# Optimization experiments

Measured on AMD Instinct MI355X. Metric: run time of the kernel, lower is better.

The kernel has to match this reference:

```python
import jax, jax.numpy as jnp
import numpy as np

WINDOW_SIZE = 16
DILATION = 2

B, L, H, E = 2, 4096, 8, 64


def setup_inputs() -> dict:
    key = jax.random.key(0)
    kq, kk, kv = jax.random.split(key, 3)
    queries = jax.random.normal(kq, (B, L, H, E), dtype=jnp.float32)
    keys = jax.random.normal(kk, (B, L, H, E), dtype=jnp.float32)
    values = jax.random.normal(kv, (B, L, H, E), dtype=jnp.float32)
    return {"queries": queries, "keys": keys, "values": values}


def _window_indices(Lk: int):
    # offsets: [-r, ..., r] * dilation ; idx[l, w] = clamp(l + off[w], 0, Lk-1)
    offsets = jnp.arange(-WINDOW_SIZE, WINDOW_SIZE + 1) * DILATION
    idx = jnp.arange(Lk)[:, None] + offsets[None, :]
    return jnp.clip(idx, 0, Lk - 1)


def reference(queries, keys, values):
    # queries/keys/values: [B, L, H, E]
    Bq, Lq, Hq, Eq = queries.shape
    scale = 1.0 / jnp.sqrt(jnp.asarray(Eq, queries.dtype))
    idx = _window_indices(keys.shape[1])
    K_win = keys[:, idx]
    V_win = values[:, idx]
    scores = jnp.einsum('blhe,blwhe->blhw', queries, K_win) * scale
    A = jax.nn.softmax(scores, axis=-1)
    V = jnp.einsum('blhw,blwhe->blhe', A, V_win)    # [B, L, H, E]
    return V
```

## Files before the change

### kernel.cpp

```cpp
#include <hip/hip_runtime.h>
#include <hip/hip_bf16.h>
#include <math.h>

#define B_    2
#define L_    4096
#define H_    8
#define E_    64
#define VTSTR 136
#define PSTR  72

using frag8 = __attribute__((ext_vector_type(8))) short;
using fl4   = __attribute__((ext_vector_type(4))) float;

__device__ __forceinline__ unsigned short f2bf(float f) {
    return __builtin_bit_cast(unsigned short, __float2bfloat16(f));
}
__device__ __forceinline__ frag8 pack8(float4 a, float4 b) {
    frag8 r;
    r[0] = (short)f2bf(a.x); r[1] = (short)f2bf(a.y);
    r[2] = (short)f2bf(a.z); r[3] = (short)f2bf(a.w);
    r[4] = (short)f2bf(b.x); r[5] = (short)f2bf(b.y);
    r[6] = (short)f2bf(b.z); r[7] = (short)f2bf(b.w);
    return r;
}

__global__ __launch_bounds__(256, 4)
void lda_kernel(const float* __restrict__ Q, const float* __restrict__ K,
                const float* __restrict__ V, float* __restrict__ O) {
    __shared__ unsigned short Vt[E_ * VTSTR];
    __shared__ unsigned short Pw[4 * 16 * PSTR];

    const int tid  = threadIdx.x;
    const int lane = tid & 63;
    const int wave = tid >> 6;
    const int col  = lane & 15;
    const int quad = lane >> 4;
    const int p    = wave & 1;
    const int t    = wave >> 1;

    const int g   = blockIdx.x;
    const int xcd = g & 7;
    const int s   = g >> 3;
    const int bh  = s & 15;
    const int xt  = (xcd << 3) | (s >> 4);
    const int l0  = xt * 64;
    const int b   = bh >> 3;
    const int h   = bh & 7;

    const size_t base = ((size_t)(b * L_) * H_ + h) * E_;
    const int    rs   = H_ * E_;

    const int lq = l0 + 2 * (16 * t + col) + p;
    frag8 aq[2];
    #pragma unroll
    for (int k = 0; k < 2; ++k) {
        const float* qp = Q + base + (size_t)lq * rs + k * 32 + quad * 8;
        aq[k] = pack8(*(const float4*)qp, *(const float4*)(qp + 4));
    }

    fl4 S[3];
    #pragma unroll
    for (int c = 0; c < 3; ++c) {
        int rhat = 16 * (t + c) + col;
        int rg = l0 - 32 + 2 * rhat + p;
        rg = rg < 0 ? 0 : (rg > L_ - 1 ? L_ - 1 : rg);
        const float* kp = K + base + (size_t)rg * rs;
        fl4 acc = {0.f, 0.f, 0.f, 0.f};
        #pragma unroll
        for (int k = 0; k < 2; ++k) {
            frag8 bk = pack8(*(const float4*)(kp + k * 32 + quad * 8),
                             *(const float4*)(kp + k * 32 + quad * 8 + 4));
            acc = __builtin_amdgcn_mfma_f32_16x16x32_bf16(aq[k], bk, acc, 0, 0, 0);
        }
        S[c] = acc;
    }

    float va[32];
    #pragma unroll
    for (int i = 0; i < 8; ++i) {
        int gi  = wave * 8 + i;
        int pg  = gi >> 4;
        int rh0 = (gi & 15) * 4;
        #pragma unroll
        for (int j = 0; j < 4; ++j) {
            int rg = l0 - 32 + 2 * (rh0 + j) + pg;
            rg = rg < 0 ? 0 : (rg > L_ - 1 ? L_ - 1 : rg);
            va[i * 4 + j] = V[base + (size_t)rg * rs + lane];
        }
    }

    float pw[3][4];
    #pragma unroll
    for (int c = 0; c < 3; ++c)
        #pragma unroll
        for (int reg = 0; reg < 4; ++reg)
            pw[c][reg] = exp2f(S[c][reg] * 0.18033688011112043f);

    const int pb = wave * 16 * PSTR;
    #pragma unroll
    for (int i = 0; i < 3; ++i) {
        int idx = lane + 64 * i;
        if (idx < 144) { uint4 z = {0u,0u,0u,0u}; *(uint4*)&Pw[pb + idx * 8] = z; }
    }
    #pragma unroll
    for (int reg = 0; reg < 4; ++reg) {
        int off = quad * 4 + reg;
        #pragma unroll
        for (int c = 0; c < 3; ++c) {
            int j = 16 * c + col - off;
            if (j >= 0 && j <= 32)
                Pw[pb + off * PSTR + 16 * (t + c) + col] = f2bf(pw[c][reg]);
        }
    }

    frag8 ap[2];
    #pragma unroll
    for (int k = 0; k < 2; ++k)
        ap[k] = *(const frag8*)&Pw[pb + col * PSTR + k * 32 + quad * 8];

    frag8 ones;
    #pragma unroll
    for (int i = 0; i < 8; ++i) ones[i] = (short)0x3F80;
    fl4 sums = {0.f, 0.f, 0.f, 0.f};
    sums = __builtin_amdgcn_mfma_f32_16x16x32_bf16(ap[0], ones, sums, 0, 0, 0);
    sums = __builtin_amdgcn_mfma_f32_16x16x32_bf16(ap[1], ones, sums, 0, 0, 0);
    float inv[4];
    #pragma unroll
    for (int reg = 0; reg < 4; ++reg) inv[reg] = __builtin_amdgcn_rcpf(sums[reg]);

    #pragma unroll
    for (int i = 0; i < 8; ++i) {
        int gi  = wave * 8 + i;
        int pg  = gi >> 4;
        int rh0 = (gi & 15) * 4;
        uint2 u;
        u.x = (unsigned)f2bf(va[i*4+0]) | ((unsigned)f2bf(va[i*4+1]) << 16);
        u.y = (unsigned)f2bf(va[i*4+2]) | ((unsigned)f2bf(va[i*4+3]) << 16);
        *(uint2*)&Vt[lane * VTSTR + pg * 64 + rh0] = u;
    }
    __syncthreads();

    #pragma unroll
    for (int nt = 0; nt < 4; ++nt) {
        fl4 c = {0.f, 0.f, 0.f, 0.f};
        #pragma unroll
        for (int k = 0; k < 2; ++k) {
            frag8 bv = *(const frag8*)&Vt[(nt * 16 + col) * VTSTR + p * 64 + k * 32 + quad * 8];
            c = __builtin_amdgcn_mfma_f32_16x16x32_bf16(ap[k], bv, c, 0, 0, 0);
        }
        #pragma unroll
        for (int reg = 0; reg < 4; ++reg) {
            int l = 2 * (16 * t + quad * 4 + reg) + p;
            __builtin_nontemporal_store(c[reg] * inv[reg],
                O + base + (size_t)(l0 + l) * rs + nt * 16 + col);
        }
    }
}

extern "C" void kernel_launch(void* const* d_in, const int* in_sizes, int n_in,
                              void* d_out, int out_size, void* d_ws, size_t ws_size,
                              hipStream_t stream) {
    const float* Q = (const float*)d_in[0];
    const float* K = (const float*)d_in[1];
    const float* V = (const float*)d_in[2];
    float* O = (float*)d_out;

    dim3 grid(L_ / 64 * B_ * H_);
    dim3 block(256);
    lda_kernel<<<grid, block, 0, stream>>>(Q, K, V, O);
}
```

Before: 91.80 us.

## Double block tile to 128 rows with 512 threads to cut V halo reloads

```diff
diff --git a/kernel.cpp b/kernel.cpp
--- a/kernel.cpp
+++ b/kernel.cpp
@@ -6,7 +6,7 @@
 #define L_    4096
 #define H_    8
 #define E_    64
-#define VTSTR 136
+#define VTSTR 200
 #define PSTR  72
 
 using frag8 = __attribute__((ext_vector_type(8))) short;
@@ -15,7 +15,7 @@
 __device__ __forceinline__ unsigned short f2bf(float f) {
     return __builtin_bit_cast(unsigned short, __float2bfloat16(f));
 }
-__device__ __forceinline__ frag8 pack8(float4 a, float4 b) {
+__device__ __forceinline__ frag8 pack8v(fl4 a, fl4 b) {
     frag8 r;
     r[0] = (short)f2bf(a.x); r[1] = (short)f2bf(a.y);
     r[2] = (short)f2bf(a.z); r[3] = (short)f2bf(a.w);
@@ -24,11 +24,11 @@
     return r;
 }
 
-__global__ __launch_bounds__(256, 4)
+__global__ __launch_bounds__(512, 2)
 void lda_kernel(const float* __restrict__ Q, const float* __restrict__ K,
                 const float* __restrict__ V, float* __restrict__ O) {
     __shared__ unsigned short Vt[E_ * VTSTR];
-    __shared__ unsigned short Pw[4 * 16 * PSTR];
+    __shared__ unsigned short Pw[8 * 16 * PSTR];
 
     const int tid  = threadIdx.x;
     const int lane = tid & 63;
@@ -42,8 +42,8 @@
     const int xcd = g & 7;
     const int s   = g >> 3;
     const int bh  = s & 15;
-    const int xt  = (xcd << 3) | (s >> 4);
-    const int l0  = xt * 64;
+    const int xt  = (xcd << 2) | (s >> 4);
+    const int l0  = xt * 128;
     const int b   = bh >> 3;
     const int h   = bh & 7;
 
@@ -55,7 +55,9 @@
     #pragma unroll
     for (int k = 0; k < 2; ++k) {
         const float* qp = Q + base + (size_t)lq * rs + k * 32 + quad * 8;
-        aq[k] = pack8(*(const float4*)qp, *(const float4*)(qp + 4));
+        fl4 qa = __builtin_nontemporal_load((const fl4*)qp);
+        fl4 qb = __builtin_nontemporal_load((const fl4*)qp + 1);
+        aq[k] = pack8v(qa, qb);
     }
 
     fl4 S[3];
@@ -68,19 +70,20 @@
         fl4 acc = {0.f, 0.f, 0.f, 0.f};
         #pragma unroll
         for (int k = 0; k < 2; ++k) {
-            frag8 bk = pack8(*(const float4*)(kp + k * 32 + quad * 8),
-                             *(const float4*)(kp + k * 32 + quad * 8 + 4));
+            frag8 bk = pack8v(*(const fl4*)(kp + k * 32 + quad * 8),
+                              *(const fl4*)(kp + k * 32 + quad * 8 + 4));
             acc = __builtin_amdgcn_mfma_f32_16x16x32_bf16(aq[k], bk, acc, 0, 0, 0);
         }
         S[c] = acc;
     }
 
-    float va[32];
+    float va[24];
     #pragma unroll
-    for (int i = 0; i < 8; ++i) {
-        int gi  = wave * 8 + i;
-        int pg  = gi >> 4;
-        int rh0 = (gi & 15) * 4;
+    for (int i = 0; i < 6; ++i) {
+        int gi  = wave * 6 + i;
+        int pg  = gi / 24;
+        int rm  = gi - pg * 24;
+        int rh0 = rm * 4;
         #pragma unroll
         for (int j = 0; j < 4; ++j) {
             int rg = l0 - 32 + 2 * (rh0 + j) + pg;
@@ -97,6 +100,7 @@
             pw[c][reg] = exp2f(S[c][reg] * 0.18033688011112043f);
 
     const int pb = wave * 16 * PSTR;
+    const int lb = 16 * (t & 1);
     #pragma unroll
     for (int i = 0; i < 3; ++i) {
         int idx = lane + 64 * i;
@@ -109,7 +113,7 @@
         for (int c = 0; c < 3; ++c) {
             int j = 16 * c + col - off;
             if (j >= 0 && j <= 32)
-                Pw[pb + off * PSTR + 16 * (t + c) + col] = f2bf(pw[c][reg]);
+                Pw[pb + off * PSTR + lb + 16 * c + col] = f2bf(pw[c][reg]);
         }
     }
 
@@ -129,30 +133,32 @@
     for (int reg = 0; reg < 4; ++reg) inv[reg] = __builtin_amdgcn_rcpf(sums[reg]);
 
     #pragma unroll
-    for (int i = 0; i < 8; ++i) {
-        int gi  = wave * 8 + i;
-        int pg  = gi >> 4;
-        int rh0 = (gi & 15) * 4;
+    for (int i = 0; i < 6; ++i) {
+        int gi  = wave * 6 + i;
+        int pg  = gi / 24;
+        int rm  = gi - pg * 24;
+        int rh0 = rm * 4;
         uint2 u;
         u.x = (unsigned)f2bf(va[i*4+0]) | ((unsigned)f2bf(va[i*4+1]) << 16);
         u.y = (unsigned)f2bf(va[i*4+2]) | ((unsigned)f2bf(va[i*4+3]) << 16);
-        *(uint2*)&Vt[lane * VTSTR + pg * 64 + rh0] = u;
+        *(uint2*)&Vt[lane * VTSTR + pg * 96 + rh0] = u;
     }
     __syncthreads();
 
+    const int rb = 32 * (t >> 1);
     #pragma unroll
     for (int nt = 0; nt < 4; ++nt) {
         fl4 c = {0.f, 0.f, 0.f, 0.f};
         #pragma unroll
         for (int k = 0; k < 2; ++k) {
-            frag8 bv = *(const frag8*)&Vt[(nt * 16 + col) * VTSTR + p * 64 + k * 32 + quad * 8];
+            frag8 bv = *(const frag8*)&Vt[(nt * 16 + col) * VTSTR + p * 96 + rb + k * 32 + quad * 8];
             c = __builtin_amdgcn_mfma_f32_16x16x32_bf16(ap[k], bv, c, 0, 0, 0);
         }
         #pragma unroll
         for (int reg = 0; reg < 4; ++reg) {
-            int l = 2 * (16 * t + quad * 4 + reg) + p;
+            int l = l0 + 2 * (16 * t + quad * 4 + reg) + p;
             __builtin_nontemporal_store(c[reg] * inv[reg],
-                O + base + (size_t)(l0 + l) * rs + nt * 16 + col);
+                O + base + (size_t)l * rs + nt * 16 + col);
         }
     }
 }
@@ -165,7 +171,7 @@
     const float* V = (const float*)d_in[2];
     float* O = (float*)d_out;
 
-    dim3 grid(L_ / 64 * B_ * H_);
-    dim3 block(256);
+    dim3 grid(L_ / 128 * B_ * H_);
+    dim3 block(512);
     lda_kernel<<<grid, block, 0, stream>>>(Q, K, V, O);
 }
```

Result: slower. 98.18 us (+7.0%).
